# Performance work log

Hardware: AMD Instinct MI355X
Metric: run time of the kernel (lower is better)

## Reference

```python
import jax, jax.numpy as jnp
import numpy as np


def setup_inputs() -> dict:
    key = jax.random.key(0)
    kq, kk, kv = jax.random.split(key, 3)
    B, HQ, HKV, S, D = 4, 32, 8, 1024, 128
    q = jax.random.normal(kq, (B, HQ, S, D), dtype=jnp.float32)
    k = jax.random.normal(kk, (B, HKV, S, D), dtype=jnp.float32)
    v = jax.random.normal(kv, (B, HKV, S, D), dtype=jnp.float32)
    return {"q": q, "k": k, "v": v, "is_causal": 1}


def reference(q, k, v, is_causal):
    # q: [B, Hq, Sq, D]; k, v: [B, Hkv, Sk, D] with Hq a multiple of Hkv (GQA).
    dtype = q.dtype
    head_size = q.shape[-1]
    scale = 1.0 / np.sqrt(head_size)  # default scale=None -> 1/sqrt(head_size_q)

    # num_head_bcast: repeat_interleave kv heads to match query heads
    rep = q.shape[1] // k.shape[1]
    k_expand = jnp.repeat(k, rep, axis=1).astype(jnp.float32)
    v_expand = jnp.repeat(v, rep, axis=1).astype(jnp.float32)
    qf = q.astype(jnp.float32)

    # materialized score matrix s: [B, Hq, Sq, Sk]
    s = jnp.einsum('bhqd,bhkd->bhqk', qf, k_expand) * scale
    if is_causal:
        sq, sk = s.shape[-2], s.shape[-1]
        causal_mask = jnp.tril(jnp.ones((sq, sk), dtype=bool))  # tril(diagonal=0)
        s = jnp.where(causal_mask, s, -jnp.inf)

    # stable softmax (matches max-subtract + softmax in the original)
    p = jax.nn.softmax(s, axis=-1)

    attn = jnp.einsum('bhqk,bhkd->bhqd', p, v_expand)
    return attn.astype(dtype)
```

## Files before the change

kernel.cpp:

```cpp
#include <hip/hip_runtime.h>
#include <hip/hip_bf16.h>

typedef __attribute__((ext_vector_type(8))) short short8;
typedef __attribute__((ext_vector_type(4))) float f32x4;
typedef __attribute__((ext_vector_type(16))) float f32x16;
typedef __attribute__((ext_vector_type(4))) unsigned int u32x4;
typedef __attribute__((ext_vector_type(2))) int i32x2;

constexpr int Bc = 4, HQc = 32, HKVc = 8, Sc = 1024, Dc = 128;
constexpr int QW = 32, QBLK = 128, KVBLK = 64, NTILE = Sc / KVBLK;
constexpr float SCALE2 = 0.08838834764831845f * 1.44269504088896340736f;
constexpr int IMG_TILE = 32768;
constexpr float MBIAS = 14.0f;

#define MFMA32(a, b, c) __builtin_amdgcn_mfma_f32_32x32x16_bf16(a, b, c, 0, 0, 0)
#define EXP2(x) __builtin_amdgcn_exp2f(x)

__device__ __forceinline__ unsigned pack2(float a, float b) {
  union { __hip_bfloat162 h2; unsigned u; } un;
  un.h2 = __float22bfloat162_rn(make_float2(a, b));
  return un.u;
}

__device__ __forceinline__ void gld_lds16(const void* g, void* l) {
  __builtin_amdgcn_global_load_lds(
      (const __attribute__((address_space(1))) void*)g,
      (__attribute__((address_space(3))) void*)l, 16, 0, 0);
}

__global__ __launch_bounds__(256, 4)
void sdpa_prep(const float* __restrict__ K, const float* __restrict__ V,
               char* __restrict__ ws)
{
  const int tid = threadIdx.x;
  const int pid = blockIdx.x;
  const int panel = pid >> 4, kt = pid & 15;
  const int b = panel >> 3, hkv = panel & 7;
  const float* Kg = K + (size_t)(b * HKVc + hkv) * Sc * Dc + (size_t)kt * KVBLK * Dc;
  const float* Vg = V + (size_t)(b * HKVc + hkv) * Sc * Dc + (size_t)kt * KVBLK * Dc;
  char* img = ws + (size_t)pid * IMG_TILE;
  const int d4 = tid & 31, k8 = tid >> 5;

#pragma unroll
  for (int it = 0; it < 4; ++it) {
    int chunk = it * 256 + tid, r = chunk >> 4, c8 = chunk & 15;
    const float* p = Kg + (size_t)r * Dc + c8 * 8;
    f32x4 f0 = *(const f32x4*)p;
    f32x4 f1 = *(const f32x4*)(p + 4);
    u32x4 w;
    w[0] = pack2(f0[0], f0[1]);
    w[1] = pack2(f0[2], f0[3]);
    w[2] = pack2(f1[0], f1[1]);
    w[3] = pack2(f1[2], f1[3]);
    int bo = r * 256 + ((c8 * 16) ^ ((r & 15) << 4));
    *(u32x4*)(img + bo) = w;
  }
  {
    f32x4 vreg[8];
#pragma unroll
    for (int rr = 0; rr < 8; ++rr)
      vreg[rr] = *(const f32x4*)(Vg + (size_t)(k8 * 8 + rr) * Dc + d4 * 4);
#pragma unroll
    for (int jj = 0; jj < 4; ++jj) {
      int d = d4 * 4 + jj;
      u32x4 w;
      w[0] = pack2(vreg[0][jj], vreg[1][jj]);
      w[1] = pack2(vreg[2][jj], vreg[3][jj]);
      w[2] = pack2(vreg[4][jj], vreg[5][jj]);
      w[3] = pack2(vreg[6][jj], vreg[7][jj]);
      int bo = 16384 + d * 128 + ((k8 * 16) ^ ((d4 & 7) << 4));
      *(u32x4*)(img + bo) = w;
    }
  }
}

__global__ __launch_bounds__(256, 3)
void sdpa_fwd(const float* __restrict__ Q, const int* __restrict__ CZ,
              float* __restrict__ O, const char* __restrict__ ws)
{
  __shared__ __align__(16) short K_lds[2][KVBLK * Dc];
  __shared__ __align__(16) short VT_lds[Dc * KVBLK];

  const int tid  = threadIdx.x;
  const int wid  = tid >> 6;
  const int lane = tid & 63;
  const int l31  = lane & 31;
  const int h    = lane >> 5;

  const int wg    = blockIdx.x;
  const int xcd   = wg & 7, t = wg >> 3;
  const int panel = (t >> 5) * 8 + xcd;
  const int b     = panel >> 3, hkv = panel & 7;
  const int u     = t & 31;
  const int qb    = 7 - (u >> 2);
  const int hh    = hkv * 4 + (u & 3);
  const int causal = CZ[0];

  const float* Qg = Q + (size_t)(b * HQc + hh) * Sc * Dc;
  float*       Og = O + (size_t)(b * HQc + hh) * Sc * Dc;
  const char*  img_panel = ws + (size_t)panel * 16 * IMG_TILE;

  const int q0w   = qb * QBLK + wid * QW;
  const int q_abs = q0w + l31;
  const int diag  = 2 * qb + (wid >> 1);
  const int nkt   = causal ? (2 * qb + 2) : NTILE;

  auto stageK = [&](int kt, int buf) {
    const char* img = img_panel + (size_t)kt * IMG_TILE;
    char* KB = (char*)K_lds[buf];
#pragma unroll
    for (int c = 0; c < 4; ++c) {
      int off = (wid * 4 + c) * 1024;
      gld_lds16(img + off + lane * 16, KB + off);
    }
  };
  auto stageV = [&](int kt) {
    const char* img = img_panel + (size_t)kt * IMG_TILE + 16384;
    char* VB = (char*)VT_lds;
#pragma unroll
    for (int c = 0; c < 4; ++c) {
      int off = (wid * 4 + c) * 1024;
      gld_lds16(img + off + lane * 16, VB + off);
    }
  };

  const int kswz = (l31 & 15) << 4, krow = l31 * 256;
  const int vswz = (l31 >> 2) << 4, vrow = l31 * 128;

  short8 qf[8];
  {
    const float* qp = Qg + (size_t)q_abs * Dc + 8 * h;
#pragma unroll
    for (int d8 = 0; d8 < 8; ++d8) {
      f32x4 f0 = *(const f32x4*)(qp + d8 * 16);
      f32x4 f1 = *(const f32x4*)(qp + d8 * 16 + 4);
      union { u32x4 u; short8 s; } t2;
      t2.u[0] = pack2(f0[0] * SCALE2, f0[1] * SCALE2);
      t2.u[1] = pack2(f0[2] * SCALE2, f0[3] * SCALE2);
      t2.u[2] = pack2(f1[0] * SCALE2, f1[1] * SCALE2);
      t2.u[3] = pack2(f1[2] * SCALE2, f1[3] * SCALE2);
      qf[d8] = t2.s;
    }
  }

  f32x16 o_acc[4];
#pragma unroll
  for (int nt = 0; nt < 4; ++nt)
#pragma unroll
    for (int rr = 0; rr < 16; ++rr) o_acc[nt][rr] = 0.f;
  float l_run = 0.f;

  typedef union { u32x4 u; short8 s; } pfrag;

  auto qk_sm = [&](int kt, int h_, int kb_buf, pfrag (&pf)[2]) {
    const char* KB = (const char*)K_lds[kb_buf];
    f32x16 sa, sb;
#pragma unroll
    for (int rr = 0; rr < 16; ++rr) { sa[rr] = 0.f; sb[rr] = 0.f; }
    const int kbase = krow + h_ * 8192;
    __builtin_amdgcn_s_setprio(1);
#pragma unroll
    for (int dd = 0; dd < 4; ++dd) {
      int cA = (32 * dd + 16 * h) ^ kswz;
      int cB = (32 * (dd + 4) + 16 * h) ^ kswz;
      short8 kfa = *(const short8*)(KB + kbase + cA);
      short8 kfb = *(const short8*)(KB + kbase + cB);
      sa = MFMA32(kfa, qf[dd], sa);
      sb = MFMA32(kfb, qf[dd + 4], sb);
    }
    __builtin_amdgcn_s_setprio(0);
    f32x16 s = sa + sb;
    if (causal && kt == diag) {
      const int kb = kt * KVBLK + h_ * 32;
#pragma unroll
      for (int rr = 0; rr < 16; ++rr) {
        int crow = (rr & 3) + 8 * (rr >> 2) + 4 * h;
        if (kb + crow > q_abs) s[rr] = -1e30f;
      }
    }
    float e8[8];
#pragma unroll
    for (int rr = 0; rr < 16; ++rr) s[rr] = EXP2(s[rr] - MBIAS);
#pragma unroll
    for (int i = 0; i < 8; ++i) e8[i] = s[2 * i] + s[2 * i + 1];
#pragma unroll
    for (int w = 4; w >= 1; w >>= 1)
#pragma unroll
      for (int i = 0; i < 4; ++i) if (i < w) e8[i] += e8[i + w];
    l_run += e8[0];
#pragma unroll
    for (int Ks = 0; Ks < 2; ++Ks) {
      const int base = 8 * Ks;
      unsigned W00 = pack2(s[base + 0], s[base + 1]);
      unsigned W20 = pack2(s[base + 2], s[base + 3]);
      unsigned W01 = pack2(s[base + 4], s[base + 5]);
      unsigned W21 = pack2(s[base + 6], s[base + 7]);
      i32x2 sA = __builtin_amdgcn_permlane32_swap((int)W00, (int)W01, false, false);
      i32x2 sB = __builtin_amdgcn_permlane32_swap((int)W20, (int)W21, false, false);
      pf[Ks].u[0] = (unsigned)sA[0];
      pf[Ks].u[1] = (unsigned)sB[0];
      pf[Ks].u[2] = (unsigned)sA[1];
      pf[Ks].u[3] = (unsigned)sB[1];
    }
  };

  auto pv = [&](int h_, pfrag (&pf)[2]) {
    const char* VB = (const char*)VT_lds;
    __builtin_amdgcn_s_setprio(1);
#pragma unroll
    for (int Ks = 0; Ks < 2; ++Ks) {
      int colx = (32 * (h_ * 2 + Ks) + 16 * h) ^ vswz;
#pragma unroll
      for (int nt = 0; nt < 4; ++nt) {
        short8 vf = *(const short8*)(VB + vrow + nt * 4096 + colx);
        o_acc[nt] = MFMA32(pf[Ks].s, vf, o_acc[nt]);
      }
    }
    __builtin_amdgcn_s_setprio(0);
  };

  stageK(0, 0);
  stageV(0);
  for (int kt = 0; kt < nkt; ++kt) {
    const int kb_buf = kt & 1;
    __syncthreads();
    if (kt > 0) stageV(kt);
    const bool act = !causal || (kt <= diag);
    const bool skip1 = (causal != 0) && (kt == diag) && ((wid & 1) == 0);
    pfrag pfA[2], pfB[2];
    if (act) qk_sm(kt, 0, kb_buf, pfA);
    if (act && !skip1) qk_sm(kt, 1, kb_buf, pfB);
    __syncthreads();
    if (kt + 1 < nkt) stageK(kt + 1, kb_buf ^ 1);
    if (act) pv(0, pfA);
    if (act && !skip1) pv(1, pfB);
  }

  float ls  = l_run + __shfl_xor(l_run, 32);
  float inv = 1.f / ls;
  float ir[16];
#pragma unroll
  for (int rr = 0; rr < 16; ++rr)
    ir[rr] = __shfl(inv, (rr & 3) + 8 * (rr >> 2) + 4 * h);
#pragma unroll
  for (int nt = 0; nt < 4; ++nt)
#pragma unroll
    for (int rr = 0; rr < 16; ++rr) {
      int qrow = q0w + (rr & 3) + 8 * (rr >> 2) + 4 * h;
      Og[(size_t)qrow * Dc + nt * 32 + l31] = o_acc[nt][rr] * ir[rr];
    }
}

extern "C" void kernel_launch(void* const* d_in, const int* in_sizes, int n_in,
                              void* d_out, int out_size, void* d_ws, size_t ws_size,
                              hipStream_t stream) {
  const float* q  = (const float*)d_in[0];
  const float* k  = (const float*)d_in[1];
  const float* v  = (const float*)d_in[2];
  const int*   cz = (const int*)d_in[3];
  float* out = (float*)d_out;
  char* ws = (char*)d_ws;
  sdpa_prep<<<dim3(512, 1, 1), 256, 0, stream>>>(k, v, ws);
  sdpa_fwd<<<dim3(1024, 1, 1), 256, 0, stream>>>(q, cz, out, ws);
}
```

Baseline: 83.05 us.

## Read V fragments directly from global workspace instead of staging through LDS

```diff
diff --git a/kernel.cpp b/kernel.cpp
--- a/kernel.cpp
+++ b/kernel.cpp
@@ -68,7 +68,7 @@
       w[1] = pack2(vreg[2][jj], vreg[3][jj]);
       w[2] = pack2(vreg[4][jj], vreg[5][jj]);
       w[3] = pack2(vreg[6][jj], vreg[7][jj]);
-      int bo = 16384 + d * 128 + ((k8 * 16) ^ ((d4 & 7) << 4));
+      int bo = 16384 + k8 * 2048 + d * 16;
       *(u32x4*)(img + bo) = w;
     }
   }
@@ -79,7 +79,6 @@
               float* __restrict__ O, const char* __restrict__ ws)
 {
   __shared__ __align__(16) short K_lds[2][KVBLK * Dc];
-  __shared__ __align__(16) short VT_lds[Dc * KVBLK];
 
   const int tid  = threadIdx.x;
   const int wid  = tid >> 6;
@@ -114,18 +113,8 @@
       gld_lds16(img + off + lane * 16, KB + off);
     }
   };
-  auto stageV = [&](int kt) {
-    const char* img = img_panel + (size_t)kt * IMG_TILE + 16384;
-    char* VB = (char*)VT_lds;
-#pragma unroll
-    for (int c = 0; c < 4; ++c) {
-      int off = (wid * 4 + c) * 1024;
-      gld_lds16(img + off + lane * 16, VB + off);
-    }
-  };
 
   const int kswz = (l31 & 15) << 4, krow = l31 * 256;
-  const int vswz = (l31 >> 2) << 4, vrow = l31 * 128;
 
   short8 qf[8];
   {
@@ -204,15 +193,14 @@
     }
   };
 
-  auto pv = [&](int h_, pfrag (&pf)[2]) {
-    const char* VB = (const char*)VT_lds;
+  auto pv = [&](const char* imgV, int h_, pfrag (&pf)[2]) {
     __builtin_amdgcn_s_setprio(1);
 #pragma unroll
     for (int Ks = 0; Ks < 2; ++Ks) {
-      int colx = (32 * (h_ * 2 + Ks) + 16 * h) ^ vswz;
+      int ks8 = 2 * (h_ * 2 + Ks) + h;
 #pragma unroll
       for (int nt = 0; nt < 4; ++nt) {
-        short8 vf = *(const short8*)(VB + vrow + nt * 4096 + colx);
+        short8 vf = *(const short8*)(imgV + ks8 * 2048 + nt * 512 + l31 * 16);
         o_acc[nt] = MFMA32(pf[Ks].s, vf, o_acc[nt]);
       }
     }
@@ -220,20 +208,16 @@
   };
 
   stageK(0, 0);
-  stageV(0);
   for (int kt = 0; kt < nkt; ++kt) {
     const int kb_buf = kt & 1;
     __syncthreads();
-    if (kt > 0) stageV(kt);
+    if (kt + 1 < nkt) stageK(kt + 1, kb_buf ^ 1);
+    const char* imgV = img_panel + (size_t)kt * IMG_TILE + 16384;
     const bool act = !causal || (kt <= diag);
     const bool skip1 = (causal != 0) && (kt == diag) && ((wid & 1) == 0);
-    pfrag pfA[2], pfB[2];
-    if (act) qk_sm(kt, 0, kb_buf, pfA);
-    if (act && !skip1) qk_sm(kt, 1, kb_buf, pfB);
-    __syncthreads();
-    if (kt + 1 < nkt) stageK(kt + 1, kb_buf ^ 1);
-    if (act) pv(0, pfA);
-    if (act && !skip1) pv(1, pfB);
+    pfrag pf[2];
+    if (act) { qk_sm(kt, 0, kb_buf, pf); pv(imgV, 0, pf); }
+    if (act && !skip1) { qk_sm(kt, 1, kb_buf, pf); pv(imgV, 1, pf); }
   }
 
   float ls  = l_run + __shfl_xor(l_run, 32);
```

Result: slower. 86.10 us (+3.7%).
